# Kernel tuning notes

Measured on AMD Instinct MI355X. Metric: run time of the kernel, lower is better.

## Reference

```python
import jax, jax.numpy as jnp
import numpy as np

# SamplesLoss('sinkhorn', p=2, blur=0.05, scaling=0.5, diameter=2.0, debias=True, backend='tensorized')
P = 2
BLUR = 0.05
SCALING = 0.5
DIAMETER = 2.0


def epsilon_schedule(p, diameter, blur, scaling):
    # geomloss epsilon annealing: diameter^p -> blur^p, geometric in eps
    eps_list = (
        [diameter ** p]
        + [np.exp(e) for e in np.arange(p * np.log(diameter), p * np.log(blur), p * np.log(scaling))]
        + [blur ** p]
    )
    return [float(e) for e in eps_list]


def softmin(eps, C, h):
    # soft C-transform: f_i = -eps * log sum_j exp(h_j - C_ij/eps)
    # C: (B,N,M), h: (B,M) -> (B,N)
    return -eps * jax.scipy.special.logsumexp(h[:, None, :] - C / eps, axis=2)


def sq_cost(x, y):
    # SqDist(x,y)/2 : (B,N,D),(B,M,D) -> (B,N,M)
    x2 = jnp.sum(x * x, axis=-1)[:, :, None]
    y2 = jnp.sum(y * y, axis=-1)[:, None, :]
    return (x2 + y2 - 2.0 * jnp.einsum('bnd,bmd->bnm', x, y)) * 0.5


def setup_inputs() -> dict:
    key = jax.random.key(0)
    k1, k2 = jax.random.split(key)
    x = jax.random.uniform(k1, (8, 2048, 3), dtype=jnp.float32)
    y = jax.random.uniform(k2, (8, 2048, 3), dtype=jnp.float32)
    return {"x": x, "y": y}


def reference(x, y):
    B, N, _ = x.shape
    M = y.shape[1]
    # uniform weights (SamplesLoss default when only point clouds are given)
    a_log = jnp.full((B, N), -float(np.log(N)), dtype=x.dtype)
    b_log = jnp.full((B, M), -float(np.log(M)), dtype=y.dtype)

    C_xy = sq_cost(x, y)                 # (B,N,M)
    C_yx = jnp.swapaxes(C_xy, 1, 2)      # (B,M,N)
    C_xx = sq_cost(x, x)                 # (B,N,N) debias term
    C_yy = sq_cost(y, y)                 # (B,M,M) debias term

    eps_list = epsilon_schedule(P, DIAMETER, BLUR, SCALING)

    # initialization at the coarsest temperature (balanced OT: damping = 1)
    eps0 = eps_list[0]
    f_aa = softmin(eps0, C_xx, a_log)
    g_bb = softmin(eps0, C_yy, b_log)
    g_ab = softmin(eps0, C_yx, a_log)
    f_ba = softmin(eps0, C_xy, b_log)

    # symmetric Sinkhorn loop with epsilon scaling (no grad tracked in torch here)
    for eps in eps_list:
        ft_ba = softmin(eps, C_xy, b_log + g_ab / eps)
        gt_ab = softmin(eps, C_yx, a_log + f_ba / eps)
        f_ba = 0.5 * (f_ba + ft_ba)
        g_ab = 0.5 * (g_ab + gt_ab)
        ft_aa = softmin(eps, C_xx, a_log + f_aa / eps)
        gt_bb = softmin(eps, C_yy, b_log + g_bb / eps)
        f_aa = 0.5 * (f_aa + ft_aa)
        g_bb = 0.5 * (g_bb + gt_bb)

    # last extrapolation step, with detached dual potentials (torch .detach())
    eps = eps_list[-1]
    sg = jax.lax.stop_gradient
    f_ba, g_ab = (
        softmin(eps, C_xy, b_log + sg(g_ab) / eps),
        softmin(eps, C_yx, a_log + sg(f_ba) / eps),
    )
    f_aa = softmin(eps, C_xx, a_log + sg(f_aa) / eps)
    g_bb = softmin(eps, C_yy, b_log + sg(g_bb) / eps)

    # debiased Sinkhorn divergence, batch mode -> (B,)
    a = jnp.exp(a_log)
    b = jnp.exp(b_log)
    return jnp.sum(a * (f_ba - f_aa), axis=-1) + jnp.sum(b * (g_ab - g_bb), axis=-1)
```

## Files before the change

### kernel.cpp

```cpp
#include <hip/hip_runtime.h>
#include <math.h>

#define BATCH 8
#define NPTS 2048
#define THREADS 256
#define HALF_COLS 1024
#define TILES_H 32
#define ROWS_PER_BLOCK 128
#define LOG_M 7.62559580411076

typedef __attribute__((ext_vector_type(8)))  __bf16 bf16x8;
typedef __attribute__((ext_vector_type(16))) float  f32x16;
typedef __attribute__((ext_vector_type(2)))  float  f32x2;

union FragU { unsigned short u[8]; uint4 v; };

__device__ __forceinline__ unsigned short f2bf(float f) {
    union { float f; unsigned u; } x; x.f = f;
    unsigned r = x.u + 0x7FFFu + ((x.u >> 16) & 1u);
    return (unsigned short)(r >> 16);
}
__device__ __forceinline__ float bf2f(unsigned short b) {
    union { unsigned u; float f; } x; x.u = ((unsigned)b) << 16;
    return x.f;
}

__global__ __launch_bounds__(THREADS, 2) void softmin_pass(
    const float* __restrict__ x, const float* __restrict__ y,
    const float* __restrict__ potSrc, float* __restrict__ potDst,
    uint4* __restrict__ CF0, uint2* __restrict__ CF1,
    float sigma, float k2, float inv_k2, float rowc0,
    int avg, int first, int last, float* __restrict__ out)
{
    __shared__ uint4 BF[TILES_H][64];
    __shared__ uint4 AF[4][64];
    __shared__ float NM[ROWS_PER_BLOCK];

    const int type  = blockIdx.z;
    const int batch = blockIdx.y;

    const float* rowP;
    const float* colP;
    int hslot, oslot, cs;
    if (type == 0)      { rowP = x; colP = y; hslot = 1; oslot = 0; cs = 1; }
    else if (type == 1) { rowP = y; colP = x; hslot = 0; oslot = 1; cs = 0; }
    else if (type == 2) { rowP = x; colP = x; hslot = 2; oslot = 2; cs = 0; }
    else                { rowP = y; colP = y; hslot = 3; oslot = 3; cs = 1; }

    rowP += batch * NPTS * 3;
    colP += batch * NPTS * 3;
    const float* hP   = potSrc + (hslot * BATCH + batch) * NPTS;
    const float* oldP = potSrc + (oslot * BATCH + batch) * NPTS;
    float*       outP = potDst + (oslot * BATCH + batch) * NPTS;
    const size_t cbase = ((size_t)cs * BATCH + batch) * NPTS;

    {
        const int gg = threadIdx.x >> 6, idx = threadIdx.x & 63;
        const int row = blockIdx.x * ROWS_PER_BLOCK + gg * 32 + (idx & 31);
        float x0 = rowP[3 * row + 0], x1 = rowP[3 * row + 1], x2 = rowP[3 * row + 2];
        float p0 = sigma * (x0 - 0.5f), p1 = sigma * (x1 - 0.5f), p2 = sigma * (x2 - 0.5f);
        unsigned short h0 = f2bf(p0); unsigned short l0 = f2bf(p0 - bf2f(h0));
        unsigned short h1 = f2bf(p1); unsigned short l1 = f2bf(p1 - bf2f(h1));
        unsigned short h2 = f2bf(p2); unsigned short l2 = f2bf(p2 - bf2f(h2));
        FragU f;
        if (idx < 32) {
            f.u[0] = h0; f.u[1] = h0; f.u[2] = l0; f.u[3] = l0;
            f.u[4] = h1; f.u[5] = h1; f.u[6] = l1; f.u[7] = l1;
        } else {
            f.u[0] = h2; f.u[1] = h2; f.u[2] = l2; f.u[3] = l2;
            f.u[4] = 0x3F80; f.u[5] = 0x3F80; f.u[6] = 0x3F80; f.u[7] = 0;
        }
        AF[gg][idx] = f.v;
    }
    if (threadIdx.x < ROWS_PER_BLOCK) {
        const int r = threadIdx.x;
        const int i = blockIdx.x * ROWS_PER_BLOCK + r;
        float x0 = rowP[3 * i + 0], x1 = rowP[3 * i + 1], x2 = rowP[3 * i + 2];
        float p0 = x0 - 0.5f, p1 = x1 - 0.5f, p2 = x2 - 0.5f;
        float rowconst = 0.5f * (p0 * p0 + p1 * p1 + p2 * p2) + rowc0;
        float oldv = first ? 0.0f : oldP[i];
        NM[r] = (oldv - rowconst) * inv_k2;
    }

    const int lane = threadIdx.x & 63;
    const int g    = threadIdx.x >> 6;
    const int khalf = lane >> 5;

    f32x2 sp[8];
    #pragma unroll
    for (int q = 0; q < 8; ++q) { sp[q].x = 0.0f; sp[q].y = 0.0f; }
    bf16x8 af;
    f32x16 nmv;

    for (int h = 0; h < 2; ++h) {
        if (h) __syncthreads();

        if (first) {
            const int writer = (blockIdx.x == 0) && (type <= 1);
            for (int jj = threadIdx.x; jj < HALF_COLS; jj += THREADS) {
                const int j = h * HALF_COLS + jj;
                float y0 = colP[3 * j + 0], y1 = colP[3 * j + 1], y2 = colP[3 * j + 2];
                float p0 = y0 - 0.5f, p1 = y1 - 0.5f, p2 = y2 - 0.5f;
                unsigned short h0 = f2bf(p0); unsigned short l0 = f2bf(p0 - bf2f(h0));
                unsigned short h1 = f2bf(p1); unsigned short l1 = f2bf(p1 - bf2f(h1));
                unsigned short h2 = f2bf(p2); unsigned short l2 = f2bf(p2 - bf2f(h2));
                float ysq = 0.5f * (p0 * p0 + p1 * p1 + p2 * p2);
                float hhe = -sigma * ysq;
                unsigned short hA = f2bf(hhe); float r1 = hhe - bf2f(hA);
                unsigned short hB = f2bf(r1);  float r2 = r1 - bf2f(hB);
                unsigned short hC = f2bf(r2);
                FragU f0, f1;
                f0.u[0] = h0; f0.u[1] = l0; f0.u[2] = h0; f0.u[3] = l0;
                f0.u[4] = h1; f0.u[5] = l1; f0.u[6] = h1; f0.u[7] = l1;
                f1.u[0] = h2; f1.u[1] = l2; f1.u[2] = h2; f1.u[3] = l2;
                f1.u[4] = hA; f1.u[5] = hB; f1.u[6] = hC; f1.u[7] = 0;
                BF[jj >> 5][jj & 31]        = f0.v;
                BF[jj >> 5][32 + (jj & 31)] = f1.v;
                if (writer) {
                    CF0[cbase + j] = f0.v;
                    CF1[cbase + j] = make_uint2(f1.v.x, __float_as_uint(ysq));
                }
            }
        } else {
            for (int jj = threadIdx.x; jj < HALF_COLS; jj += THREADS) {
                const int j = h * HALF_COLS + jj;
                uint4 f0  = CF0[cbase + j];
                uint2 f1l = CF1[cbase + j];
                float ysq = __uint_as_float(f1l.y);
                float hhe = sigma * (hP[j] - ysq);
                unsigned short hA = f2bf(hhe); float r1 = hhe - bf2f(hA);
                unsigned short hB = f2bf(r1);  float r2 = r1 - bf2f(hB);
                unsigned short hC = f2bf(r2);
                uint4 f1 = make_uint4(f1l.x, f1l.x,
                                      (unsigned)hA | ((unsigned)hB << 16),
                                      (unsigned)hC);
                BF[jj >> 5][jj & 31]        = f0;
                BF[jj >> 5][32 + (jj & 31)] = f1;
            }
        }
        __syncthreads();

        if (h == 0) {
            af = *(const bf16x8*)&AF[g][lane];
            #pragma unroll
            for (int r = 0; r < 16; ++r) {
                const int row = (r & 3) + 8 * (r >> 2) + 4 * khalf;
                nmv[r] = NM[g * 32 + row];
            }
        }

        #pragma unroll 2
        for (int t = 0; t < TILES_H; ++t) {
            bf16x8 bf = *(const bf16x8*)&BF[t][lane];
            f32x16 acc = __builtin_amdgcn_mfma_f32_32x32x16_bf16(af, bf, nmv, 0, 0, 0);
            #pragma unroll
            for (int q = 0; q < 8; ++q) {
                f32x2 e;
                e.x = __builtin_amdgcn_exp2f(acc[2 * q]);
                e.y = __builtin_amdgcn_exp2f(acc[2 * q + 1]);
                asm("v_pk_add_f32 %0, %0, %1" : "+v"(sp[q]) : "v"(e));
            }
        }
    }

    __syncthreads();
    {
        f32x2* SP = (f32x2*)&BF[0][0];
        #pragma unroll
        for (int q = 0; q < 8; ++q)
            SP[(q * 4 + g) * 64 + (lane ^ ((q & 3) << 3))] = sp[q];
    }
    __syncthreads();

    {
        const float* SPf = (const float*)&BF[0][0];
        const int v  = threadIdx.x >> 1;
        const int p  = threadIdx.x & 1;
        const int gg = v >> 5, vv = v & 31;
        const int kh = (vv >> 2) & 1;
        const int r  = (vv & 3) | ((vv >> 3) << 2);
        const int q  = r >> 1, comp = r & 1;
        const int sw = (q & 3) << 3;
        float val = 0.0f;
        #pragma unroll
        for (int jj = 0; jj < 16; ++jj) {
            const int j = (p * 16 + jj + v) & 31;
            const int l = kh * 32 + j;
            val += SPf[(((q * 4 + gg) * 64) + (l ^ sw)) * 2 + comp];
        }
        val += __shfl_xor(val, 1, 64);
        if (p == 0) {
            const int i = blockIdx.x * ROWS_PER_BLOCK + v;
            float oldv = first ? 0.0f : oldP[i];
            float res  = oldv - k2 * __log2f(val);
            outP[i] = avg ? 0.5f * (oldv + res) : res;
            if (last) NM[v] = res;
        }
    }

    if (last) {
        __syncthreads();
        if (g == 0) {
            float v2 = NM[lane] + NM[64 + lane];
            #pragma unroll
            for (int off = 32; off >= 1; off >>= 1)
                v2 += __shfl_xor(v2, off, 64);
            if (lane == 0) {
                float sign = (type >= 2) ? -1.0f : 1.0f;
                atomicAdd(out + batch, sign * v2 * (1.0f / NPTS));
            }
        }
    }
}

extern "C" void kernel_launch(void* const* d_in, const int* in_sizes, int n_in,
                              void* d_out, int out_size, void* d_ws, size_t ws_size,
                              hipStream_t stream)
{
    const float* x = (const float*)d_in[0];
    const float* y = (const float*)d_in[1];
    float* out = (float*)d_out;

    const size_t potElems = (size_t)4 * BATCH * NPTS;
    const size_t colElems = (size_t)2 * BATCH * NPTS;
    float* P0  = (float*)d_ws;
    float* P1  = P0 + potElems;
    uint4* CF0 = (uint4*)(P1 + potElems);
    uint2* CF1 = (uint2*)(CF0 + colElems);

    hipMemsetAsync(out, 0, BATCH * sizeof(float), stream);

    double epsl[16];
    int ne = 0;
    epsl[ne++] = 4.0;
    const double stop = 2.0 * log(0.05);
    const double step = 2.0 * log(0.5);
    for (double e = 2.0 * log(2.0); e > stop; e += step)
        epsl[ne++] = exp(e);
    epsl[ne++] = 0.05 * 0.05;

    float* src = P0;
    float* dst = P1;
    dim3 grid(NPTS / ROWS_PER_BLOCK, BATCH, 4);

    auto launch = [&](double eps, int avg, int first, int last) {
        float sigma  = (float)(M_LOG2E / eps);
        float k2     = (float)(eps * M_LN2);
        float inv_k2 = (float)(1.0 / (eps * M_LN2));
        float rowc0  = (float)(eps * LOG_M);
        softmin_pass<<<grid, THREADS, 0, stream>>>(
            x, y, src, dst, CF0, CF1,
            sigma, k2, inv_k2, rowc0, avg, first, last, out);
        float* t = src; src = dst; dst = t;
    };

    launch(epsl[0], 0, 1, 0);
    for (int k = 0; k < ne; ++k)
        launch(epsl[k], 1, 0, 0);
    launch(epsl[ne - 1], 0, 0, 1);
}
```

Baseline: 232.5 us.

## Merge xy/yx softmin passes by accumulating column sums from the row exponentials

Measured after the change: 241.7 us. 1.04x slower.

```diff
diff --git a/kernel.cpp b/kernel.cpp
--- a/kernel.cpp
+++ b/kernel.cpp
@@ -6,7 +6,8 @@
 #define THREADS 256
 #define HALF_COLS 1024
 #define TILES_H 32
-#define ROWS_PER_BLOCK 128
+#define CROWS 128
+#define MROWS 64
 #define LOG_M 7.62559580411076
 
 typedef __attribute__((ext_vector_type(8)))  __bf16 bf16x8;
@@ -25,19 +26,27 @@
     return x.f;
 }
 
-__global__ __launch_bounds__(THREADS, 2) void softmin_pass(
+
+__global__ __launch_bounds__(THREADS, 2) void softmin_classic(
     const float* __restrict__ x, const float* __restrict__ y,
     const float* __restrict__ potSrc, float* __restrict__ potDst,
     uint4* __restrict__ CF0, uint2* __restrict__ CF1,
-    float sigma, float k2, float inv_k2, float rowc0,
+    const float* __restrict__ gPrev, const float* __restrict__ rPrev,
+    float* __restrict__ gDst, float* __restrict__ zeroR,
+    float sigma, float k2, float inv_k2, float rowc0, float prevHalfK2,
     int avg, int first, int last, float* __restrict__ out)
 {
     __shared__ uint4 BF[TILES_H][64];
     __shared__ uint4 AF[4][64];
-    __shared__ float NM[ROWS_PER_BLOCK];
+    __shared__ float NM[CROWS];
 
     const int type  = blockIdx.z;
     const int batch = blockIdx.y;
+
+    if (zeroR) {
+        const int lid = ((blockIdx.z * gridDim.y + blockIdx.y) * gridDim.x + blockIdx.x);
+        if (threadIdx.x < 32) zeroR[lid * 32 + threadIdx.x] = 0.0f;
+    }
 
     const float* rowP;
     const float* colP;
@@ -54,9 +63,15 @@
     float*       outP = potDst + (oslot * BATCH + batch) * NPTS;
     const size_t cbase = ((size_t)cs * BATCH + batch) * NPTS;
 
+    const bool  fixH = (rPrev != nullptr) && (hslot == 1);
+    const bool  fixO = (rPrev != nullptr) && (oslot == 1);
+    const float* gB  = gPrev + batch * NPTS;
+    const float* rB  = rPrev + batch * NPTS;
+    float* gW = (gDst != nullptr && oslot == 1) ? (gDst + batch * NPTS) : nullptr;
+
     {
         const int gg = threadIdx.x >> 6, idx = threadIdx.x & 63;
-        const int row = blockIdx.x * ROWS_PER_BLOCK + gg * 32 + (idx & 31);
+        const int row = blockIdx.x * CROWS + gg * 32 + (idx & 31);
         float x0 = rowP[3 * row + 0], x1 = rowP[3 * row + 1], x2 = rowP[3 * row + 2];
         float p0 = sigma * (x0 - 0.5f), p1 = sigma * (x1 - 0.5f), p2 = sigma * (x2 - 0.5f);
         unsigned short h0 = f2bf(p0); unsigned short l0 = f2bf(p0 - bf2f(h0));
@@ -72,13 +87,14 @@
         }
         AF[gg][idx] = f.v;
     }
-    if (threadIdx.x < ROWS_PER_BLOCK) {
+    if (threadIdx.x < CROWS) {
         const int r = threadIdx.x;
-        const int i = blockIdx.x * ROWS_PER_BLOCK + r;
+        const int i = blockIdx.x * CROWS + r;
         float x0 = rowP[3 * i + 0], x1 = rowP[3 * i + 1], x2 = rowP[3 * i + 2];
         float p0 = x0 - 0.5f, p1 = x1 - 0.5f, p2 = x2 - 0.5f;
         float rowconst = 0.5f * (p0 * p0 + p1 * p1 + p2 * p2) + rowc0;
-        float oldv = first ? 0.0f : oldP[i];
+        float oldv = first ? 0.0f
+                   : (fixO ? (gB[i] - prevHalfK2 * __log2f(rB[i])) : oldP[i]);
         NM[r] = (oldv - rowconst) * inv_k2;
     }
 
@@ -127,7 +143,8 @@
                 uint4 f0  = CF0[cbase + j];
                 uint2 f1l = CF1[cbase + j];
                 float ysq = __uint_as_float(f1l.y);
-                float hhe = sigma * (hP[j] - ysq);
+                float hpj = fixH ? (gB[j] - prevHalfK2 * __log2f(rB[j])) : hP[j];
+                float hhe = sigma * (hpj - ysq);
                 unsigned short hA = f2bf(hhe); float r1 = hhe - bf2f(hA);
                 unsigned short hB = f2bf(r1);  float r2 = r1 - bf2f(hB);
                 unsigned short hC = f2bf(r2);
@@ -190,10 +207,12 @@
         }
         val += __shfl_xor(val, 1, 64);
         if (p == 0) {
-            const int i = blockIdx.x * ROWS_PER_BLOCK + v;
-            float oldv = first ? 0.0f : oldP[i];
+            const int i = blockIdx.x * CROWS + v;
+            float oldv = first ? 0.0f
+                       : (fixO ? (gB[i] - prevHalfK2 * __log2f(rB[i])) : oldP[i]);
             float res  = oldv - k2 * __log2f(val);
             outP[i] = avg ? 0.5f * (oldv + res) : res;
+            if (gW) gW[i] = res;
             if (last) NM[v] = res;
         }
     }
@@ -209,6 +228,194 @@
                 float sign = (type >= 2) ? -1.0f : 1.0f;
                 atomicAdd(out + batch, sign * v2 * (1.0f / NPTS));
             }
+        }
+    }
+}
+
+__global__ __launch_bounds__(THREADS, 2) void softmin_merged(
+    const float* __restrict__ x, const float* __restrict__ y,
+    const float* __restrict__ potSrc, float* __restrict__ potDst,
+    const uint4* __restrict__ CF0, const uint2* __restrict__ CF1,
+    const float* __restrict__ gPrev, const float* __restrict__ rPrev,
+    float* __restrict__ gDst, float* __restrict__ rCur, float* __restrict__ rZero,
+    float sigma, float k2, float inv_k2, float rowc0, float prevHalfK2)
+{
+    __shared__ uint4 BF[TILES_H][64];
+    __shared__ uint4 AF[2][64];
+    __shared__ float NM[MROWS];
+    __shared__ float CS[HALF_COLS];
+
+    const int type  = blockIdx.z;
+    const int batch = blockIdx.y;
+    const int doCol = (type == 0);
+
+    const float* rowP; const float* colP;
+    int oslot, hslot, cs;
+    if (type == 0)      { rowP = x; colP = y; oslot = 0; hslot = 0; cs = 1; }
+    else if (type == 1) { rowP = x; colP = x; oslot = 2; hslot = 2; cs = 0; }
+    else                { rowP = y; colP = y; oslot = 3; hslot = 3; cs = 1; }
+
+    rowP += batch * NPTS * 3;
+    colP += batch * NPTS * 3;
+    const float* hP   = potSrc + (hslot * BATCH + batch) * NPTS;
+    const float* oldP = potSrc + (oslot * BATCH + batch) * NPTS;
+    float*       outP = potDst + (oslot * BATCH + batch) * NPTS;
+    const size_t cbase = ((size_t)cs * BATCH + batch) * NPTS;
+    const int gb = batch * NPTS;
+    const int writer = doCol && (blockIdx.x == 0);
+
+    if (doCol) {
+        for (int c0 = threadIdx.x; c0 < HALF_COLS; c0 += THREADS) CS[c0] = 0.0f;
+        const int zb = (batch * 32 + blockIdx.x) * 64;
+        if (threadIdx.x < 64) rZero[zb + threadIdx.x] = 0.0f;
+    }
+
+    if (threadIdx.x < 128) {
+        const int gg = threadIdx.x >> 6, idx = threadIdx.x & 63;
+        const int row = blockIdx.x * MROWS + gg * 32 + (idx & 31);
+        float x0 = rowP[3 * row + 0], x1 = rowP[3 * row + 1], x2 = rowP[3 * row + 2];
+        float p0 = sigma * (x0 - 0.5f), p1 = sigma * (x1 - 0.5f), p2 = sigma * (x2 - 0.5f);
+        unsigned short h0 = f2bf(p0); unsigned short l0 = f2bf(p0 - bf2f(h0));
+        unsigned short h1 = f2bf(p1); unsigned short l1 = f2bf(p1 - bf2f(h1));
+        unsigned short h2 = f2bf(p2); unsigned short l2 = f2bf(p2 - bf2f(h2));
+        FragU f;
+        if (idx < 32) {
+            f.u[0] = h0; f.u[1] = h0; f.u[2] = l0; f.u[3] = l0;
+            f.u[4] = h1; f.u[5] = h1; f.u[6] = l1; f.u[7] = l1;
+        } else {
+            f.u[0] = h2; f.u[1] = h2; f.u[2] = l2; f.u[3] = l2;
+            f.u[4] = 0x3F80; f.u[5] = 0x3F80; f.u[6] = 0x3F80; f.u[7] = 0;
+        }
+        AF[gg][idx] = f.v;
+    } else if (threadIdx.x < 128 + MROWS) {
+        const int r = threadIdx.x - 128;
+        const int i = blockIdx.x * MROWS + r;
+        float x0 = rowP[3 * i + 0], x1 = rowP[3 * i + 1], x2 = rowP[3 * i + 2];
+        float p0 = x0 - 0.5f, p1 = x1 - 0.5f, p2 = x2 - 0.5f;
+        float rowconst = 0.5f * (p0 * p0 + p1 * p1 + p2 * p2) + rowc0;
+        NM[r] = (oldP[i] - rowconst) * inv_k2;
+    }
+
+    const int lane = threadIdx.x & 63;
+    const int wave = threadIdx.x >> 6;
+    const int g    = wave >> 1;
+    const int c    = wave & 1;
+    const int khalf = lane >> 5;
+
+    f32x2 sp[8];
+    #pragma unroll
+    for (int q = 0; q < 8; ++q) { sp[q].x = 0.0f; sp[q].y = 0.0f; }
+    bf16x8 af;
+    f32x16 nmv;
+
+    for (int h = 0; h < 2; ++h) {
+        if (h) {
+            __syncthreads();
+            if (doCol) {
+                for (int c0 = threadIdx.x; c0 < HALF_COLS; c0 += THREADS) {
+                    atomicAdd(&rCur[gb + c0], CS[c0]);
+                    CS[c0] = 0.0f;
+                }
+            }
+        }
+
+        for (int jj = threadIdx.x; jj < HALF_COLS; jj += THREADS) {
+            const int j = h * HALF_COLS + jj;
+            uint4 f0  = CF0[cbase + j];
+            uint2 f1l = CF1[cbase + j];
+            float ysq = __uint_as_float(f1l.y);
+            float hpj;
+            if (doCol) {
+                hpj = gPrev[gb + j];
+                if (rPrev) hpj -= prevHalfK2 * __log2f(rPrev[gb + j]);
+                if (writer) gDst[gb + j] = hpj;
+            } else {
+                hpj = hP[j];
+            }
+            float hhe = sigma * (hpj - ysq);
+            unsigned short hA = f2bf(hhe); float r1 = hhe - bf2f(hA);
+            unsigned short hB = f2bf(r1);  float r2 = r1 - bf2f(hB);
+            unsigned short hC = f2bf(r2);
+            uint4 f1 = make_uint4(f1l.x, f1l.x,
+                                  (unsigned)hA | ((unsigned)hB << 16),
+                                  (unsigned)hC);
+            BF[jj >> 5][jj & 31]        = f0;
+            BF[jj >> 5][32 + (jj & 31)] = f1;
+        }
+        __syncthreads();
+
+        if (h == 0) {
+            af = *(const bf16x8*)&AF[g][lane];
+            #pragma unroll
+            for (int r = 0; r < 16; ++r) {
+                const int row = (r & 3) + 8 * (r >> 2) + 4 * khalf;
+                nmv[r] = NM[g * 32 + row];
+            }
+        }
+
+        const int tbase = c * (TILES_H / 2);
+        #pragma unroll 2
+        for (int t = 0; t < TILES_H / 2; ++t) {
+            bf16x8 bf = *(const bf16x8*)&BF[tbase + t][lane];
+            f32x16 acc = __builtin_amdgcn_mfma_f32_32x32x16_bf16(af, bf, nmv, 0, 0, 0);
+            f32x2 ct; ct.x = 0.0f; ct.y = 0.0f;
+            #pragma unroll
+            for (int q = 0; q < 8; ++q) {
+                f32x2 e;
+                e.x = __builtin_amdgcn_exp2f(acc[2 * q]);
+                e.y = __builtin_amdgcn_exp2f(acc[2 * q + 1]);
+                asm("v_pk_add_f32 %0, %0, %1" : "+v"(sp[q]) : "v"(e));
+                if (doCol)
+                    asm("v_pk_add_f32 %0, %0, %1" : "+v"(ct) : "v"(e));
+            }
+            if (doCol) {
+                float cv = ct.x + ct.y;
+                cv += __shfl_xor(cv, 32, 64);
+                if (lane < 32) atomicAdd(&CS[(tbase + t) * 32 + lane], cv);
+            }
+        }
+    }
+
+    __syncthreads();
+    if (doCol) {
+        for (int c0 = threadIdx.x; c0 < HALF_COLS; c0 += THREADS)
+            atomicAdd(&rCur[gb + HALF_COLS + c0], CS[c0]);
+    }
+    {
+        f32x2* SP = (f32x2*)&BF[0][0];
+        #pragma unroll
+        for (int q = 0; q < 8; ++q)
+            SP[(q * 4 + wave) * 64 + (lane ^ ((q & 3) << 3))] = sp[q];
+    }
+    __syncthreads();
+
+    {
+        const float* SPf = (const float*)&BF[0][0];
+        const int v  = threadIdx.x >> 2;
+        const int p  = threadIdx.x & 3;
+        const int gg = v >> 5, vv = v & 31;
+        const int kh = (vv >> 2) & 1;
+        const int r  = (vv & 3) | ((vv >> 3) << 2);
+        const int q  = r >> 1, comp = r & 1;
+        const int sw = (q & 3) << 3;
+        float val = 0.0f;
+        #pragma unroll
+        for (int cc = 0; cc < 2; ++cc) {
+            const int w = gg * 2 + cc;
+            #pragma unroll
+            for (int jj = 0; jj < 8; ++jj) {
+                const int j = p * 8 + ((jj + v) & 7);
+                const int l = kh * 32 + j;
+                val += SPf[(((q * 4 + w) * 64) + (l ^ sw)) * 2 + comp];
+            }
+        }
+        val += __shfl_xor(val, 1, 64);
+        val += __shfl_xor(val, 2, 64);
+        if (p == 0) {
+            const int i = blockIdx.x * MROWS + v;
+            float oldv = oldP[i];
+            float res  = oldv - k2 * __log2f(val);
+            outP[i] = 0.5f * (oldv + res);
         }
     }
 }
@@ -223,10 +430,15 @@
 
     const size_t potElems = (size_t)4 * BATCH * NPTS;
     const size_t colElems = (size_t)2 * BATCH * NPTS;
+    const size_t bn       = (size_t)BATCH * NPTS;
     float* P0  = (float*)d_ws;
     float* P1  = P0 + potElems;
     uint4* CF0 = (uint4*)(P1 + potElems);
     uint2* CF1 = (uint2*)(CF0 + colElems);
+    float* Gb  = (float*)(CF1 + colElems);
+    float* Rb  = Gb + 2 * bn;
+    float* G[2] = { Gb, Gb + bn };
+    float* R[3] = { Rb, Rb + bn, Rb + 2 * bn };
 
     hipMemsetAsync(out, 0, BATCH * sizeof(float), stream);
 
@@ -241,21 +453,38 @@
 
     float* src = P0;
     float* dst = P1;
-    dim3 grid(NPTS / ROWS_PER_BLOCK, BATCH, 4);
-
-    auto launch = [&](double eps, int avg, int first, int last) {
-        float sigma  = (float)(M_LOG2E / eps);
-        float k2     = (float)(eps * M_LN2);
-        float inv_k2 = (float)(1.0 / (eps * M_LN2));
-        float rowc0  = (float)(eps * LOG_M);
-        softmin_pass<<<grid, THREADS, 0, stream>>>(
+    dim3 gridC(NPTS / CROWS, BATCH, 4);
+    dim3 gridM(NPTS / MROWS, BATCH, 3);
+
+    auto sig = [](double eps) { return (float)(M_LOG2E / eps); };
+    auto kk2 = [](double eps) { return (float)(eps * M_LN2); };
+    auto ik2 = [](double eps) { return (float)(1.0 / (eps * M_LN2)); };
+    auto rc0 = [](double eps) { return (float)(eps * LOG_M); };
+
+    softmin_classic<<<gridC, THREADS, 0, stream>>>(
+        x, y, src, dst, CF0, CF1,
+        nullptr, nullptr, G[0], R[1],
+        sig(epsl[0]), kk2(epsl[0]), ik2(epsl[0]), rc0(epsl[0]), 0.0f,
+        0, 1, 0, out);
+    { float* t = src; src = dst; dst = t; }
+    double prevEps = epsl[0];
+
+    for (int k = 1; k <= ne; ++k) {
+        double eps = epsl[k - 1];
+        softmin_merged<<<gridM, THREADS, 0, stream>>>(
             x, y, src, dst, CF0, CF1,
-            sigma, k2, inv_k2, rowc0, avg, first, last, out);
-        float* t = src; src = dst; dst = t;
-    };
-
-    launch(epsl[0], 0, 1, 0);
-    for (int k = 0; k < ne; ++k)
-        launch(epsl[k], 1, 0, 0);
-    launch(epsl[ne - 1], 0, 0, 1);
+            G[(k - 1) & 1], (k >= 2) ? R[(k - 1) % 3] : nullptr, G[k & 1],
+            R[k % 3], R[(k + 1) % 3],
+            sig(eps), kk2(eps), ik2(eps), rc0(eps),
+            (float)(0.5 * prevEps * M_LN2));
+        { float* t = src; src = dst; dst = t; }
+        prevEps = eps;
+    }
+
+    softmin_classic<<<gridC, THREADS, 0, stream>>>(
+        x, y, src, dst, CF0, CF1,
+        G[ne & 1], R[ne % 3], nullptr, nullptr,
+        sig(epsl[ne - 1]), kk2(epsl[ne - 1]), ik2(epsl[ne - 1]), rc0(epsl[ne - 1]),
+        (float)(0.5 * prevEps * M_LN2),
+        0, 0, 1, out);
 }
```
